# Kernel tuning notes

Hardware: AMD Instinct MI355X
Metric: run time of the kernel (lower is better)

Reference implementation:

```python
import jax, jax.numpy as jnp
import numpy as np

EPS = 1e-5
DIM_HEAD = 64
HEADS = 16
SCALE = DIM_HEAD ** -0.5


def rotate_half(x):
    # '... (j d) -> ... j d' with j=2, then (-x2, x1)
    x = x.reshape(*x.shape[:-1], 2, x.shape[-1] // 2)
    x1, x2 = x[..., 0, :], x[..., 1, :]
    return jnp.concatenate((-x2, x1), axis=-1)


def apply_rotary(freqs, t):
    # freqs: (n, rot_dim) broadcasts against t: (b, h, n, d)
    rot_dim = freqs.shape[-1]
    t_rot, t_pass = t[..., :rot_dim], t[..., rot_dim:]
    t_rot = t_rot * jnp.cos(freqs) + rotate_half(t_rot) * jnp.sin(freqs)
    return jnp.concatenate((t_rot, t_pass), axis=-1)


def setup_inputs() -> dict:
    key = jax.random.key(0)
    ks = jax.random.split(key, 4)
    b, n, dim = 2, 2048, 1024
    inner = HEADS * DIM_HEAD
    x = jax.random.normal(ks[0], (b, n, dim), dtype=jnp.float32)
    mask = jnp.ones((b, n), dtype=bool)
    rotary_pos_emb = jax.random.normal(ks[1], (n, 32), dtype=jnp.float32)
    W_qkv = jax.random.normal(ks[2], (dim, inner * 3), dtype=jnp.float32) * (dim ** -0.5)
    W_out = jax.random.normal(ks[3], (inner, dim), dtype=jnp.float32) * (inner ** -0.5)
    gamma = jnp.ones((dim,), dtype=jnp.float32)
    return {"x": x, "mask": mask, "rotary_pos_emb": rotary_pos_emb,
            "W_qkv": W_qkv, "W_out": W_out, "gamma": gamma}


def reference(x, mask, rotary_pos_emb, W_qkv, W_out, gamma):
    b, n, _ = x.shape
    qkv = x @ W_qkv  # (b, n, 3*inner)
    q, k, v = jnp.split(qkv, 3, axis=-1)
    def split_heads(t):
        return t.reshape(b, n, HEADS, DIM_HEAD).transpose(0, 2, 1, 3)  # b h n d
    q, k, v = map(split_heads, (q, k, v))
    q = q * SCALE
    q = apply_rotary(rotary_pos_emb, q)
    k = apply_rotary(rotary_pos_emb, k)
    v = apply_rotary(rotary_pos_emb, v)
    sim = jnp.einsum('bhid,bhjd->bhij', q, k)
    mask_value = -jnp.finfo(sim.dtype).max
    sim = jnp.where(mask[:, None, None, :], sim, mask_value)
    sim = sim - jax.lax.stop_gradient(jnp.max(sim, axis=-1, keepdims=True))
    attn = jax.nn.softmax(sim, axis=-1)
    out = jnp.einsum('bhij,bhjd->bhid', attn, v)
    out = out.transpose(0, 2, 1, 3).reshape(b, n, HEADS * DIM_HEAD)
    out = out @ W_out
    # LayerNorm with learned gamma, zero beta
    mean = jnp.mean(out, axis=-1, keepdims=True)
    var = jnp.var(out, axis=-1, keepdims=True)
    out = (out - mean) * jax.lax.rsqrt(var + EPS) * gamma
    return out
```

## Files before the change

kernel.cpp:

```cpp
#include <hip/hip_runtime.h>

typedef __attribute__((ext_vector_type(8))) short s16x8;
typedef __attribute__((ext_vector_type(4))) float f32x4;

#define AS1q __attribute__((address_space(1)))
#define AS3q __attribute__((address_space(3)))

__device__ __forceinline__ void gload16(const void* g, void* l) {
  __builtin_amdgcn_global_load_lds((const AS1q unsigned int*)g,
                                   (AS3q unsigned int*)l, 16, 0, 0);
}

__device__ __forceinline__ unsigned short f2bf(float f) {
  unsigned int u = __float_as_uint(f);
  u = (u + 0x7FFFu + ((u >> 16) & 1u)) >> 16;
  return (unsigned short)u;
}

__device__ __forceinline__ float bf2f(unsigned short u) {
  return __uint_as_float(((unsigned int)u) << 16);
}

__device__ __forceinline__ unsigned int cvtpk(float a, float b) {
  unsigned int r;
  asm("v_cvt_pk_bf16_f32 %0, %1, %2" : "=v"(r) : "v"(a), "v"(b));
  return r;
}

__global__ __launch_bounds__(256) void prep_kernel(
    const float* __restrict__ rope, float* __restrict__ cosT, float* __restrict__ sinT,
    const float* __restrict__ x, unsigned short* __restrict__ xb,
    const float* __restrict__ Wqkv, unsigned short* __restrict__ wqT,
    const float* __restrict__ Wout, unsigned short* __restrict__ woT) {
  __shared__ float tile[32][33];
  int bid = blockIdx.x, t = threadIdx.x;
  if (bid < 256) {
    int i = bid * 256 + t;
    float f = rope[i];
    cosT[i] = cosf(f);
    sinT[i] = sinf(f);
  } else if (bid < 4352) {
    int i = ((bid - 256) * 256 + t) * 4;
    float4 v = *(const float4*)(x + i);
    ushort4 o;
    o.x = f2bf(v.x); o.y = f2bf(v.y); o.z = f2bf(v.z); o.w = f2bf(v.w);
    *(ushort4*)(xb + i) = o;
  } else {
    const float* in; unsigned short* out; int N, lin;
    if (bid < 7424) { in = Wqkv; out = wqT; N = 3072; lin = bid - 4352; }
    else            { in = Wout; out = woT; N = 1024; lin = bid - 7424; }
    int k0 = (lin & 31) * 32, n0 = (lin >> 5) * 32;
    int tx = t & 31, ty = t >> 5;
    #pragma unroll
    for (int r = ty; r < 32; r += 8) tile[r][tx] = in[(size_t)(k0 + r) * N + n0 + tx];
    __syncthreads();
    #pragma unroll
    for (int r = ty; r < 32; r += 8) out[(size_t)(n0 + r) * 1024 + k0 + tx] = f2bf(tile[tx][r]);
  }
}

__global__ __launch_bounds__(256) void gemm_bt_bf16(
    const unsigned short* __restrict__ A, const unsigned short* __restrict__ Bt,
    unsigned short* __restrict__ C, int M, int N, int K, int nbn, int chunk) {
  __shared__ alignas(16) unsigned short Al[2][128 * 64];
  __shared__ alignas(16) unsigned short Bl[2][128 * 64];
  int tid = threadIdx.x, w = tid >> 6, l = tid & 63;
  int l16 = l & 15, lg = l >> 4;
  int lin = (blockIdx.x & 7) * chunk + (blockIdx.x >> 3);
  int m0 = (lin / nbn) * 128, n0 = (lin % nbn) * 128;
  f32x4 acc[4][4] = {};
  int srow0 = w * 8 + (l >> 3);
  int sblk = l & 7;
  auto STAGE = [&](int buf, int k0) {
    #pragma unroll
    for (int c = 0; c < 4; c++) {
      int row = c * 32 + srow0;
      gload16((const char*)A + ((size_t)(m0 + row) * K + k0) * 2 + ((sblk ^ (row & 7)) * 16),
              (char*)Al[buf] + c * 4096 + w * 1024);
      gload16((const char*)Bt + ((size_t)(n0 + row) * K + k0) * 2 + ((sblk ^ (row & 7)) * 16),
              (char*)Bl[buf] + c * 4096 + w * 1024);
    }
  };
  STAGE(0, 0);
  __syncthreads();
  int cur = 0;
  for (int k0 = 0; k0 < K; k0 += 64) {
    if (k0 + 64 < K) STAGE(cur ^ 1, k0 + 64);
    const char* Ac = (const char*)Al[cur];
    const char* Bc = (const char*)Bl[cur];
    #pragma unroll
    for (int kk = 0; kk < 2; kk++) {
      s16x8 af[4], bf[4];
      #pragma unroll
      for (int i = 0; i < 4; i++) {
        int ar = (w >> 1) * 64 + i * 16 + l16;
        int ab = ar * 128 + (kk * 32 + 8 * lg) * 2; ab ^= (ar & 7) << 4;
        af[i] = *(const s16x8*)(Ac + ab);
        int br = (w & 1) * 64 + i * 16 + l16;
        int bb = br * 128 + (kk * 32 + 8 * lg) * 2; bb ^= (br & 7) << 4;
        bf[i] = *(const s16x8*)(Bc + bb);
      }
      #pragma unroll
      for (int i = 0; i < 4; i++)
        #pragma unroll
        for (int j = 0; j < 4; j++)
          acc[i][j] = __builtin_amdgcn_mfma_f32_16x16x32_bf16(af[i], bf[j], acc[i][j], 0, 0, 0);
    }
    __syncthreads();
    cur ^= 1;
  }
  #pragma unroll
  for (int i = 0; i < 4; i++)
    #pragma unroll
    for (int j = 0; j < 4; j++)
      #pragma unroll
      for (int r = 0; r < 4; r++) {
        int mrow = m0 + (w >> 1) * 64 + i * 16 + 4 * lg + r;
        int ncol = n0 + (w & 1) * 64 + j * 16 + l16;
        C[(size_t)mrow * N + ncol] = f2bf(acc[i][j][r]);
      }
}

__global__ __launch_bounds__(256) void gemm_qkv(
    const unsigned short* __restrict__ A, const unsigned short* __restrict__ Bt,
    const float* __restrict__ cosT, const float* __restrict__ sinT,
    unsigned short* __restrict__ Qb, unsigned short* __restrict__ Kb,
    unsigned short* __restrict__ Vb, int K) {
  __shared__ alignas(16) char smem[65536];
  float (*cs)[68] = (float(*)[68])smem;
  int tid = threadIdx.x, w = tid >> 6, l = tid & 63;
  int l16 = l & 15, lg = l >> 4;
  int lin = (blockIdx.x & 7) * 96 + (blockIdx.x >> 3);
  int m0 = (lin / 24) * 128, n0 = (lin % 24) * 128;
  f32x4 acc[4][4] = {};
  int srow0 = w * 8 + (l >> 3);
  int sblk = l & 7;
  auto STAGE = [&](int buf, int k0) {
    char* Ad = smem + buf * 16384;
    char* Bd = smem + 32768 + buf * 16384;
    #pragma unroll
    for (int c = 0; c < 4; c++) {
      int row = c * 32 + srow0;
      gload16((const char*)A + ((size_t)(m0 + row) * K + k0) * 2 + ((sblk ^ (row & 7)) * 16),
              Ad + c * 4096 + w * 1024);
      gload16((const char*)Bt + ((size_t)(n0 + row) * K + k0) * 2 + ((sblk ^ (row & 7)) * 16),
              Bd + c * 4096 + w * 1024);
    }
  };
  STAGE(0, 0);
  __syncthreads();
  int cur = 0;
  for (int k0 = 0; k0 < K; k0 += 64) {
    if (k0 + 64 < K) STAGE(cur ^ 1, k0 + 64);
    const char* Ac = smem + cur * 16384;
    const char* Bc = smem + 32768 + cur * 16384;
    #pragma unroll
    for (int kk = 0; kk < 2; kk++) {
      s16x8 af[4], bf[4];
      #pragma unroll
      for (int i = 0; i < 4; i++) {
        int ar = (w >> 1) * 64 + i * 16 + l16;
        int ab = ar * 128 + (kk * 32 + 8 * lg) * 2; ab ^= (ar & 7) << 4;
        af[i] = *(const s16x8*)(Ac + ab);
        int br = (w & 1) * 64 + i * 16 + l16;
        int bb = br * 128 + (kk * 32 + 8 * lg) * 2; bb ^= (br & 7) << 4;
        bf[i] = *(const s16x8*)(Bc + bb);
      }
      #pragma unroll
      for (int i = 0; i < 4; i++)
        #pragma unroll
        for (int j = 0; j < 4; j++)
          acc[i][j] = __builtin_amdgcn_mfma_f32_16x16x32_bf16(af[i], bf[j], acc[i][j], 0, 0, 0);
    }
    __syncthreads();
    cur ^= 1;
  }
  int b = m0 >> 11;
  int nnb = m0 & 2047;
  for (int g = tid; g < 128 * 16; g += 256) {
    int row = g >> 4;
    int c4 = (g & 15) * 4;
    float4 val;
    if (c4 < 32) val = *(const float4*)(cosT + (size_t)(nnb + row) * 32 + c4);
    else         val = *(const float4*)(sinT + (size_t)(nnb + row) * 32 + (c4 - 32));
    *(float4*)&cs[row][c4] = val;
  }
  __syncthreads();
  int section = n0 >> 10;
  int h = ((n0 & 1023) >> 6) + (w & 1);
  unsigned short* dst = section == 0 ? Qb : (section == 1 ? Kb : Vb);
  float scl = section == 0 ? 0.18033688011112042f : 1.0f;
  #pragma unroll
  for (int i = 0; i < 4; i++)
    #pragma unroll
    for (int r = 0; r < 4; r++) {
      int lrow = (w >> 1) * 64 + i * 16 + 4 * lg + r;
      float c0 = cs[lrow][l16],      s0 = cs[lrow][32 + l16];
      float c1 = cs[lrow][16 + l16], s1 = cs[lrow][48 + l16];
      float a0 = acc[i][0][r], a1 = acc[i][1][r];
      float o0 = (c0 * a0 - s0 * a1) * scl;
      float o1 = (c1 * a1 + s1 * a0) * scl;
      float o2 = acc[i][2][r] * scl;
      float o3 = acc[i][3][r] * scl;
      int nn = nnb + lrow;
      size_t obase = ((size_t)(b * 16 + h) * 2048 + nn) * 64;
      dst[obase + l16]      = f2bf(o0);
      dst[obase + 16 + l16] = f2bf(o1);
      dst[obase + 32 + l16] = f2bf(o2);
      dst[obase + 48 + l16] = f2bf(o3);
    }
}

__global__ __launch_bounds__(256) void vtrans_kernel(const unsigned short* __restrict__ Vb,
                                                     unsigned short* __restrict__ Vt) {
  __shared__ unsigned short vt[64][65];
  int nb = blockIdx.x, bh = blockIdx.y;
  int t = threadIdx.x;
  int nl = t >> 2, quarter = t & 3;
  size_t src = ((size_t)bh * 2048 + nb * 64 + nl) * 64 + quarter * 16;
  s16x8 v0 = *(const s16x8*)(Vb + src);
  s16x8 v1 = *(const s16x8*)(Vb + src + 8);
  #pragma unroll
  for (int i = 0; i < 8; i++) {
    vt[nl][quarter * 16 + i] = (unsigned short)v0[i];
    vt[nl][quarter * 16 + 8 + i] = (unsigned short)v1[i];
  }
  __syncthreads();
  int drow = t >> 2;
  size_t dstb = ((size_t)bh * 64 + drow) * 2048 + (size_t)nb * 64 + (size_t)quarter * 16;
  s16x8 o0, o1;
  #pragma unroll
  for (int j = 0; j < 8; j++) {
    int p = quarter * 16 + j;
    int c = 32 * (p >> 5) + 16 * ((p >> 2) & 1) + 4 * ((p >> 3) & 3) + (p & 3);
    o0[j] = (short)vt[c][drow];
  }
  #pragma unroll
  for (int j = 0; j < 8; j++) {
    int p = quarter * 16 + 8 + j;
    int c = 32 * (p >> 5) + 16 * ((p >> 2) & 1) + 4 * ((p >> 3) & 3) + (p & 3);
    o1[j] = (short)vt[c][drow];
  }
  *(s16x8*)(Vt + dstb) = o0;
  *(s16x8*)(Vt + dstb + 8) = o1;
}

__global__ __launch_bounds__(256) void flash_kernel(
    const unsigned short* __restrict__ Q, const unsigned short* __restrict__ K,
    const unsigned short* __restrict__ Vt, unsigned short* __restrict__ A2) {
  __shared__ alignas(16) unsigned short Kl[2][128 * 64];
  __shared__ alignas(16) unsigned short Vl[2][2][64 * 64];
  int id = blockIdx.x;
  int s = id >> 3;
  int bh = (id & 7) * 4 + (s >> 4);
  int qblk = s & 15;
  int tid = threadIdx.x, w = tid >> 6, l = tid & 63;
  int l16 = l & 15, lg = l >> 4;
  size_t base = (size_t)bh * 2048 * 64;
  const unsigned short* Qb = Q + base;
  const unsigned short* Kb = K + base;
  const unsigned short* Vb = Vt + base;
  int q0 = qblk * 128 + w * 16;
  s16x8 qfA[2], qfB[2];
  {
    const s16x8* qpA = (const s16x8*)(Qb + (size_t)(q0 + l16) * 64);
    qfA[0] = qpA[lg]; qfA[1] = qpA[lg + 4];
    const s16x8* qpB = (const s16x8*)(Qb + (size_t)(q0 + 64 + l16) * 64);
    qfB[0] = qpB[lg]; qfB[1] = qpB[lg + 4];
  }
  s16x8 ones;
  #pragma unroll
  for (int i = 0; i < 8; i++) ones[i] = (short)0x3F80;
  f32x4 oA[4], oB[4], o5A, o5B;
  {
    f32x4 z = {0.f, 0.f, 0.f, 0.f};
    #pragma unroll
    for (int nd = 0; nd < 4; nd++) { oA[nd] = z; oB[nd] = z; }
    o5A = z; o5B = z;
  }
  int srow0 = w * 8 + (l >> 3);
  int sblk = l & 7;
  auto STAGE = [&](int buf, int t0) {
    #pragma unroll
    for (int c = 0; c < 4; c++) {
      int row = c * 32 + srow0;
      gload16((const char*)Kb + (size_t)(t0 + row) * 128 + ((sblk ^ (row & 7)) * 16),
              (char*)Kl[buf] + c * 4096 + w * 1024);
    }
    #pragma unroll
    for (int s2 = 0; s2 < 2; s2++)
      #pragma unroll
      for (int c = 0; c < 2; c++) {
        int row = c * 32 + srow0;
        gload16((const char*)Vb + (size_t)row * 4096 + (size_t)(t0 + s2 * 64) * 2 + ((sblk ^ (row & 7)) * 16),
                (char*)Vl[buf][s2] + c * 4096 + w * 1024);
      }
  };
  STAGE(0, 0);
  __syncthreads();
  int cur = 0;
  for (int t0 = 0; t0 < 2048; t0 += 128) {
    if (t0 + 128 < 2048) STAGE(cur ^ 1, t0 + 128);
    #pragma unroll
    for (int sub = 0; sub < 2; sub++) {
      const char* Kc = (const char*)Kl[cur] + sub * 8192;
      const char* Vc = (const char*)Vl[cur][sub];
      f32x4 sfA[4], sfB[4];
      __builtin_amdgcn_s_setprio(1);
      #pragma unroll
      for (int nbt = 0; nbt < 4; nbt++) {
        f32x4 z = {0.f, 0.f, 0.f, 0.f};
        sfA[nbt] = z; sfB[nbt] = z;
        #pragma unroll
        for (int kk = 0; kk < 2; kk++) {
          int kvrow = nbt * 16 + l16;
          int byte_ = kvrow * 128 + (kk * 32 + 8 * lg) * 2;
          byte_ ^= (kvrow & 7) << 4;
          s16x8 bfr = *(const s16x8*)(Kc + byte_);
          sfA[nbt] = __builtin_amdgcn_mfma_f32_16x16x32_bf16(bfr, qfA[kk], sfA[nbt], 0, 0, 0);
          sfB[nbt] = __builtin_amdgcn_mfma_f32_16x16x32_bf16(bfr, qfB[kk], sfB[nbt], 0, 0, 0);
        }
      }
      __builtin_amdgcn_s_setprio(0);
      s16x8 paA0, paA1, paB0, paB1;
      {
        float e0[4], e1[4], e2[4], e3[4];
        #pragma unroll
        for (int r = 0; r < 4; r++) {
          e0[r] = __builtin_amdgcn_exp2f(sfA[0][r]);
          e1[r] = __builtin_amdgcn_exp2f(sfA[1][r]);
          e2[r] = __builtin_amdgcn_exp2f(sfA[2][r]);
          e3[r] = __builtin_amdgcn_exp2f(sfA[3][r]);
        }
        unsigned int* w0 = (unsigned int*)&paA0;
        unsigned int* w1 = (unsigned int*)&paA1;
        w0[0] = cvtpk(e0[0], e0[1]); w0[1] = cvtpk(e0[2], e0[3]);
        w0[2] = cvtpk(e1[0], e1[1]); w0[3] = cvtpk(e1[2], e1[3]);
        w1[0] = cvtpk(e2[0], e2[1]); w1[1] = cvtpk(e2[2], e2[3]);
        w1[2] = cvtpk(e3[0], e3[1]); w1[3] = cvtpk(e3[2], e3[3]);
      }
      {
        float e0[4], e1[4], e2[4], e3[4];
        #pragma unroll
        for (int r = 0; r < 4; r++) {
          e0[r] = __builtin_amdgcn_exp2f(sfB[0][r]);
          e1[r] = __builtin_amdgcn_exp2f(sfB[1][r]);
          e2[r] = __builtin_amdgcn_exp2f(sfB[2][r]);
          e3[r] = __builtin_amdgcn_exp2f(sfB[3][r]);
        }
        unsigned int* w0 = (unsigned int*)&paB0;
        unsigned int* w1 = (unsigned int*)&paB1;
        w0[0] = cvtpk(e0[0], e0[1]); w0[1] = cvtpk(e0[2], e0[3]);
        w0[2] = cvtpk(e1[0], e1[1]); w0[3] = cvtpk(e1[2], e1[3]);
        w1[0] = cvtpk(e2[0], e2[1]); w1[1] = cvtpk(e2[2], e2[3]);
        w1[2] = cvtpk(e3[0], e3[1]); w1[3] = cvtpk(e3[2], e3[3]);
      }
      __builtin_amdgcn_s_setprio(1);
      #pragma unroll
      for (int nk = 0; nk < 2; nk++) {
        s16x8 pA = nk ? paA1 : paA0;
        s16x8 pB = nk ? paB1 : paB0;
        #pragma unroll
        for (int nd = 0; nd < 4; nd++) {
          int drow = nd * 16 + l16;
          int vb = drow * 128 + (nk * 32 + 8 * lg) * 2;
          vb ^= (drow & 7) << 4;
          s16x8 vfr = *(const s16x8*)(Vc + vb);
          oA[nd] = __builtin_amdgcn_mfma_f32_16x16x32_bf16(pA, vfr, oA[nd], 0, 0, 0);
          oB[nd] = __builtin_amdgcn_mfma_f32_16x16x32_bf16(pB, vfr, oB[nd], 0, 0, 0);
        }
        o5A = __builtin_amdgcn_mfma_f32_16x16x32_bf16(pA, ones, o5A, 0, 0, 0);
        o5B = __builtin_amdgcn_mfma_f32_16x16x32_bf16(pB, ones, o5B, 0, 0, 0);
      }
      __builtin_amdgcn_s_setprio(0);
    }
    __syncthreads();
    cur ^= 1;
  }
  float rsA[4], rsB[4];
  #pragma unroll
  for (int r = 0; r < 4; r++) {
    rsA[r] = __builtin_amdgcn_rcpf(o5A[r]);
    rsB[r] = __builtin_amdgcn_rcpf(o5B[r]);
  }
  int b = bh >> 4, h = bh & 15;
  #pragma unroll
  for (int nd = 0; nd < 4; nd++)
    #pragma unroll
    for (int r = 0; r < 4; r++) {
      int qA = q0 + 4 * lg + r;
      int d = nd * 16 + l16;
      A2[((size_t)(b * 2048 + qA)) * 1024 + h * 64 + d] = f2bf(oA[nd][r] * rsA[r]);
      A2[((size_t)(b * 2048 + qA + 64)) * 1024 + h * 64 + d] = f2bf(oB[nd][r] * rsB[r]);
    }
}

__global__ __launch_bounds__(256) void ln_kernel(const unsigned short* __restrict__ in,
    const float* __restrict__ gamma, float* __restrict__ out) {
  __shared__ float red[8];
  int row = blockIdx.x, t = threadIdx.x;
  const unsigned short* r = in + (size_t)row * 1024;
  ushort4 u4 = *(const ushort4*)(r + t * 4);
  float4 v;
  v.x = bf2f(u4.x); v.y = bf2f(u4.y); v.z = bf2f(u4.z); v.w = bf2f(u4.w);
  float s = v.x + v.y + v.z + v.w;
  float s2 = v.x * v.x + v.y * v.y + v.z * v.z + v.w * v.w;
  #pragma unroll
  for (int off = 1; off < 64; off <<= 1) { s += __shfl_xor(s, off); s2 += __shfl_xor(s2, off); }
  if ((t & 63) == 0) { red[t >> 6] = s; red[4 + (t >> 6)] = s2; }
  __syncthreads();
  float S = red[0] + red[1] + red[2] + red[3];
  float S2 = red[4] + red[5] + red[6] + red[7];
  float mean = S * (1.f / 1024.f);
  float var = S2 * (1.f / 1024.f) - mean * mean;
  float inv = rsqrtf(var + 1e-5f);
  float4 g = *(const float4*)(gamma + t * 4);
  float4 ov;
  ov.x = (v.x - mean) * inv * g.x;
  ov.y = (v.y - mean) * inv * g.y;
  ov.z = (v.z - mean) * inv * g.z;
  ov.w = (v.w - mean) * inv * g.w;
  *(float4*)(out + (size_t)row * 1024 + t * 4) = ov;
}

extern "C" void kernel_launch(void* const* d_in, const int* in_sizes, int n_in,
                              void* d_out, int out_size, void* d_ws, size_t ws_size,
                              hipStream_t stream) {
  const float* x     = (const float*)d_in[0];
  const float* rope  = (const float*)d_in[2];
  const float* Wqkv  = (const float*)d_in[3];
  const float* Wout  = (const float*)d_in[4];
  const float* gamma = (const float*)d_in[5];
  float* out = (float*)d_out;

  char* ws = (char*)d_ws;
  unsigned short* Qb  = (unsigned short*)(ws + 0);
  unsigned short* Kb  = (unsigned short*)(ws + 8388608);
  unsigned short* Vb  = (unsigned short*)(ws + 16777216);
  unsigned short* Vt  = (unsigned short*)(ws + 25165824);
  unsigned short* out2= (unsigned short*)(ws + 33554432);
  unsigned short* xb  = (unsigned short*)(ws + 50331648);
  unsigned short* wqT = (unsigned short*)(ws + 58720256);
  unsigned short* woT = (unsigned short*)(ws + 65011712);
  float*          cosT= (float*)(ws + 67108864);
  float*          sinT= (float*)(ws + 67371008);
  unsigned short* a2 = xb;

  prep_kernel<<<8448, 256, 0, stream>>>(rope, cosT, sinT, x, xb, Wqkv, wqT, Wout, woT);
  gemm_qkv<<<768, 256, 0, stream>>>(xb, wqT, cosT, sinT, Qb, Kb, Vb, 1024);
  vtrans_kernel<<<dim3(32, 32), 256, 0, stream>>>(Vb, Vt);
  flash_kernel<<<512, 256, 0, stream>>>(Qb, Kb, Vt, a2);
  gemm_bt_bf16<<<256, 256, 0, stream>>>(a2, woT, out2, 4096, 1024, 1024, 8, 32);
  ln_kernel<<<4096, 256, 0, stream>>>(out2, gamma, out);
}
```

Baseline: 119.0 us.

## Widen QKV GEMM tile to 128x192 with six waves per block

The QKV projection GEMM now uses 128x192 output tiles computed by six waves (2x3) instead of 128x128 tiles with four waves. The grid drops from 768 to 512 blocks and LDS grows to 80KB through dynamic shared memory. Staging loads are redistributed across 384 threads, and the epilogue maps each wave to its own head. The aim is better reuse of the A tile and an even block count across CUs, at the cost of higher LDS use per block, which may limit occupancy.

Measured after the change: 122.8 us. +3.2%, slower.

```diff
diff --git a/kernel.cpp b/kernel.cpp
--- a/kernel.cpp
+++ b/kernel.cpp
@@ -121,30 +121,33 @@
       }
 }
 
-__global__ __launch_bounds__(256) void gemm_qkv(
+__global__ __launch_bounds__(384) void gemm_qkv(
     const unsigned short* __restrict__ A, const unsigned short* __restrict__ Bt,
     const float* __restrict__ cosT, const float* __restrict__ sinT,
     unsigned short* __restrict__ Qb, unsigned short* __restrict__ Kb,
     unsigned short* __restrict__ Vb, int K) {
-  __shared__ alignas(16) char smem[65536];
+  extern __shared__ char smem[];
   float (*cs)[68] = (float(*)[68])smem;
-  int tid = threadIdx.x, w = tid >> 6, l = tid & 63;
+  int tid = threadIdx.x, w = tid / 64, l = tid & 63;
   int l16 = l & 15, lg = l >> 4;
-  int lin = (blockIdx.x & 7) * 96 + (blockIdx.x >> 3);
-  int m0 = (lin / 24) * 128, n0 = (lin % 24) * 128;
+  int wr = w >= 3 ? 1 : 0, wc = w - wr * 3;
+  int lin = (blockIdx.x & 7) * 64 + (blockIdx.x >> 3);
+  int m0 = (lin >> 4) * 128, n0 = (lin & 15) * 192;
   f32x4 acc[4][4] = {};
-  int srow0 = w * 8 + (l >> 3);
-  int sblk = l & 7;
   auto STAGE = [&](int buf, int k0) {
     char* Ad = smem + buf * 16384;
-    char* Bd = smem + 32768 + buf * 16384;
-    #pragma unroll
-    for (int c = 0; c < 4; c++) {
-      int row = c * 32 + srow0;
-      gload16((const char*)A + ((size_t)(m0 + row) * K + k0) * 2 + ((sblk ^ (row & 7)) * 16),
-              Ad + c * 4096 + w * 1024);
-      gload16((const char*)Bt + ((size_t)(n0 + row) * K + k0) * 2 + ((sblk ^ (row & 7)) * 16),
-              Bd + c * 4096 + w * 1024);
+    char* Bd = smem + 32768 + buf * 24576;
+    for (int sg = tid; sg < 2560; sg += 384) {
+      if (sg < 1024) {
+        int row = sg >> 3, blk = sg & 7;
+        gload16((const char*)A + ((size_t)(m0 + row) * K + k0) * 2 + ((blk ^ (row & 7)) * 16),
+                Ad + (sg & ~63) * 16);
+      } else {
+        int s2 = sg - 1024;
+        int row = s2 >> 3, blk = s2 & 7;
+        gload16((const char*)Bt + ((size_t)(n0 + row) * K + k0) * 2 + ((blk ^ (row & 7)) * 16),
+                Bd + (s2 & ~63) * 16);
+      }
     }
   };
   STAGE(0, 0);
@@ -153,16 +156,16 @@
   for (int k0 = 0; k0 < K; k0 += 64) {
     if (k0 + 64 < K) STAGE(cur ^ 1, k0 + 64);
     const char* Ac = smem + cur * 16384;
-    const char* Bc = smem + 32768 + cur * 16384;
+    const char* Bc = smem + 32768 + cur * 24576;
     #pragma unroll
     for (int kk = 0; kk < 2; kk++) {
       s16x8 af[4], bf[4];
       #pragma unroll
       for (int i = 0; i < 4; i++) {
-        int ar = (w >> 1) * 64 + i * 16 + l16;
+        int ar = wr * 64 + i * 16 + l16;
         int ab = ar * 128 + (kk * 32 + 8 * lg) * 2; ab ^= (ar & 7) << 4;
         af[i] = *(const s16x8*)(Ac + ab);
-        int br = (w & 1) * 64 + i * 16 + l16;
+        int br = wc * 64 + i * 16 + l16;
         int bb = br * 128 + (kk * 32 + 8 * lg) * 2; bb ^= (br & 7) << 4;
         bf[i] = *(const s16x8*)(Bc + bb);
       }
@@ -177,7 +180,7 @@
   }
   int b = m0 >> 11;
   int nnb = m0 & 2047;
-  for (int g = tid; g < 128 * 16; g += 256) {
+  for (int g = tid; g < 128 * 16; g += 384) {
     int row = g >> 4;
     int c4 = (g & 15) * 4;
     float4 val;
@@ -186,15 +189,16 @@
     *(float4*)&cs[row][c4] = val;
   }
   __syncthreads();
-  int section = n0 >> 10;
-  int h = ((n0 & 1023) >> 6) + (w & 1);
+  int nw0 = n0 + wc * 64;
+  int section = nw0 >> 10;
+  int h = (nw0 & 1023) >> 6;
   unsigned short* dst = section == 0 ? Qb : (section == 1 ? Kb : Vb);
   float scl = section == 0 ? 0.18033688011112042f : 1.0f;
   #pragma unroll
   for (int i = 0; i < 4; i++)
     #pragma unroll
     for (int r = 0; r < 4; r++) {
-      int lrow = (w >> 1) * 64 + i * 16 + 4 * lg + r;
+      int lrow = wr * 64 + i * 16 + 4 * lg + r;
       float c0 = cs[lrow][l16],      s0 = cs[lrow][32 + l16];
       float c1 = cs[lrow][16 + l16], s1 = cs[lrow][48 + l16];
       float a0 = acc[i][0][r], a1 = acc[i][1][r];
@@ -446,8 +450,15 @@
   float*          sinT= (float*)(ws + 67371008);
   unsigned short* a2 = xb;
 
+  static bool attr_set = false;
+  if (!attr_set) {
+    hipFuncSetAttribute((const void*)gemm_qkv,
+                        hipFuncAttributeMaxDynamicSharedMemorySize, 81920);
+    attr_set = true;
+  }
+
   prep_kernel<<<8448, 256, 0, stream>>>(rope, cosT, sinT, x, xb, Wqkv, wqT, Wout, woT);
-  gemm_qkv<<<768, 256, 0, stream>>>(xb, wqT, cosT, sinT, Qb, Kb, Vb, 1024);
+  gemm_qkv<<<512, 384, 81920, stream>>>(xb, wqT, cosT, sinT, Qb, Kb, Vb, 1024);
   vtrans_kernel<<<dim3(32, 32), 256, 0, stream>>>(Vb, Vt);
   flash_kernel<<<512, 256, 0, stream>>>(Qb, Kb, Vt, a2);
   gemm_bt_bf16<<<256, 256, 0, stream>>>(a2, woT, out2, 4096, 1024, 1024, 8, 32);
```
